# Kernel optimization log

Hardware: AMD Instinct MI355X
Metric: run time of the kernel (lower is better)

Reference implementation:

```python
import jax, jax.numpy as jnp
import numpy as np

B, H, NI, NT, D = 512, 1, 36, 50, 1024
NEG = -1e9
EPS = 1e-8

def setup_inputs() -> dict:
    key = jax.random.key(0)
    ks = jax.random.split(key, 12)
    s = 1.0 / np.sqrt(D)
    return {
        "imgE": jax.random.normal(ks[0], (B, H, NI, D), jnp.float32),
        "txtE": jax.random.normal(ks[1], (B, H, NT, D), jnp.float32),
        "x_mask": jax.random.randint(ks[2], (B, H, 1, NI), 0, 2).astype(bool),
        "y_mask": jax.random.randint(ks[3], (B, H, 1, NT), 0, 2).astype(bool),
        "W_img": jax.random.uniform(ks[4], (D, D), jnp.float32, -s, s),
        "b_img": jax.random.uniform(ks[5], (D,), jnp.float32, -s, s),
        "W_txt": jax.random.uniform(ks[6], (D, D), jnp.float32, -s, s),
        "b_txt": jax.random.uniform(ks[7], (D,), jnp.float32, -s, s),
        "W_img1": jax.random.uniform(ks[8], (D, D), jnp.float32, -s, s),
        "b_img1": jax.random.uniform(ks[9], (D,), jnp.float32, -s, s),
        "W_txt1": jax.random.uniform(ks[10], (D, D), jnp.float32, -s, s),
        "b_txt1": jax.random.uniform(ks[11], (D,), jnp.float32, -s, s),
    }

def reference(imgE, txtE, x_mask, y_mask,
              W_img, b_img, W_txt, b_txt, W_img1, b_img1, W_txt1, b_txt1):
    # projections
    x = jnp.einsum('bhnd,de->bhne', imgE, W_img) + b_img   # [B,H,NI,D]
    y = jnp.einsum('bhmd,de->bhme', txtE, W_txt) + b_txt   # [B,H,NT,D]
    # cosine-normalized attention scores [B,H,NI,NT]
    att = jnp.einsum('bhnd,bhmd->bhnm', x, y)
    wx = jnp.linalg.norm(x, axis=-1)[..., :, None]          # [B,H,NI,1]
    wy = jnp.linalg.norm(y, axis=-1)[..., None, :]          # [B,H,1,NT]
    att = att / jnp.maximum(wx * wy, EPS)
    # img <- txt direction
    att1 = jax.nn.softmax(jnp.where(y_mask, NEG, att), axis=-1)
    att_x = jnp.einsum('bhnm,bhmd->bhnd', att1, txtE)
    gate_x = jax.nn.sigmoid(att_x * imgE)
    fuse_x = jnp.einsum('bhnd,de->bhne', gate_x * att_x, W_img1) + b_img1
    img_out = fuse_x + imgE
    # txt <- img direction
    att2 = jax.nn.softmax(jnp.where(x_mask, NEG, jnp.swapaxes(att, 2, 3)), axis=-1)
    att_y = jnp.einsum('bhmn,bhnd->bhmd', att2, imgE)
    gate_y = jax.nn.sigmoid(att_y * txtE)
    fuse_y = jnp.einsum('bhmd,de->bhme', gate_y * att_y, W_txt1) + b_txt1
    txt_out = fuse_y + txtE
    return (img_out, txt_out)
```

## Files before the change

kernel.cpp:

```cpp
#include <hip/hip_runtime.h>

typedef unsigned short u16;
typedef unsigned int u32;
typedef __attribute__((ext_vector_type(8))) short sv8;
typedef __attribute__((ext_vector_type(4))) float fv4;

__device__ __forceinline__ u16 f2b(float f) {
  u32 u = __builtin_bit_cast(u32, f);
  u32 r = (u + 0x7fffu + ((u >> 16) & 1u)) >> 16;
  return (u16)r;
}
__device__ __forceinline__ float b2f(u16 h) {
  return __builtin_bit_cast(float, ((u32)h) << 16);
}
__device__ __forceinline__ void gld16(const void* g, void* l) {
  __builtin_amdgcn_global_load_lds(
      (const __attribute__((address_space(1))) u32*)g,
      (__attribute__((address_space(3))) u32*)l, 16, 0, 0);
}

__global__ __launch_bounds__(256) void cast_k(const float4* __restrict__ in,
                                              u16* __restrict__ out, int n4) {
  int i = blockIdx.x * 256 + threadIdx.x;
  const int stride = gridDim.x * 256;
  for (; i < n4; i += stride) {
    float4 v = in[i];
    u32 p0 = (u32)f2b(v.x) | ((u32)f2b(v.y) << 16);
    u32 p1 = (u32)f2b(v.z) | ((u32)f2b(v.w) << 16);
    uint2 o; o.x = p0; o.y = p1;
    ((uint2*)out)[i] = o;
  }
}

__global__ __launch_bounds__(256) void wtrans_k(const float* __restrict__ W0,
                                                const float* __restrict__ W1,
                                                const float* __restrict__ W2,
                                                const float* __restrict__ W3,
                                                u16* __restrict__ out) {
  const int z = blockIdx.z;
  const float* W = (z == 0) ? W0 : (z == 1) ? W1 : (z == 2) ? W2 : W3;
  u16* o = out + (size_t)z * 1048576;
  __shared__ float t[32][33];
  const int tid = threadIdx.x;
  const int r = tid >> 5, cc = tid & 31;
  const int d0 = blockIdx.x * 32, e0 = blockIdx.y * 32;
#pragma unroll
  for (int i = 0; i < 4; ++i)
    t[r + i * 8][cc] = W[(size_t)(d0 + r + i * 8) * 1024 + e0 + cc];
  __syncthreads();
#pragma unroll
  for (int i = 0; i < 4; ++i) {
    int row = r + i * 8;
    o[(size_t)(e0 + row) * 1024 + d0 + cc] = f2b(t[cc][row]);
  }
}

template <int MODE>
__global__ __launch_bounds__(512, 4) void gemm2_k(
    const u16* __restrict__ Aimg, const u16* __restrict__ Atxt,
    const u16* __restrict__ Wimg, const u16* __restrict__ Wtxt,
    const float* __restrict__ bii, const float* __restrict__ btt,
    const float* __restrict__ rii, const float* __restrict__ rtt,
    u16* __restrict__ obi, u16* __restrict__ obt,
    float* __restrict__ ofi, float* __restrict__ oft) {
  __shared__ __attribute__((aligned(16))) char smem[65536];
  const int tid = threadIdx.x;
  const int lane = tid & 63;
  const int w = tid >> 6;
  const int wm = w >> 2, wn = w & 3;
  const int l15 = lane & 15, l4 = lane >> 4;
  const int lin = blockIdx.y * 8 + blockIdx.x;
  const int xcd = lin & 7, slot = lin >> 3;
  const int bcol0 = (slot & 7) * 128;
  const int prow = xcd + ((slot >> 3) << 3);

  const char* Ab; const char* Bb; const float* bias; const float* resid;
  u16* ob; float* of; int brow0;
  if (prow < 144) {
    brow0 = prow * 128;
    Ab = (const char*)Aimg + (size_t)brow0 * 2048;
    Bb = (const char*)Wimg + (size_t)bcol0 * 2048;
    bias = bii; resid = rii; ob = obi; of = ofi;
  } else {
    brow0 = (prow - 144) * 128;
    Ab = (const char*)Atxt + (size_t)brow0 * 2048;
    Bb = (const char*)Wtxt + (size_t)bcol0 * 2048;
    bias = btt; resid = rtt; ob = obt; of = oft;
  }
  const int wr = wm * 64;
  const int wc = wn * 32;
  fv4 acc[4][2] = {};

  const int srow = tid >> 3;
  const int schunk = tid & 7;

  auto STAGE = [&](int bb, int k0) {
    char* base = smem + bb * 32768;
#pragma unroll
    for (int i = 0; i < 2; ++i) {
      int row = i * 64 + srow;
      int g = schunk ^ (row & 7);
      gld16(Ab + (size_t)row * 2048 + k0 * 2 + g * 16,
            base + i * 8192 + tid * 16);
    }
#pragma unroll
    for (int i = 0; i < 2; ++i) {
      int row = i * 64 + srow;
      int g = schunk ^ (row & 7);
      gld16(Bb + (size_t)row * 2048 + k0 * 2 + g * 16,
            base + 16384 + i * 8192 + tid * 16);
    }
  };

  STAGE(0, 0);
  for (int t = 0; t < 16; ++t) {
    const int cur = t & 1;
    if (t < 15) {
      STAGE(cur ^ 1, (t + 1) * 64);
      asm volatile("s_waitcnt vmcnt(4)" ::: "memory");
    } else {
      asm volatile("s_waitcnt vmcnt(0)" ::: "memory");
    }
    __builtin_amdgcn_s_barrier();
    __builtin_amdgcn_sched_barrier(0);
    const char* Al = smem + cur * 32768;
    const char* Bl = Al + 16384;
#pragma unroll
    for (int ks = 0; ks < 2; ++ks) {
      sv8 af[4], bf[2];
#pragma unroll
      for (int m = 0; m < 4; ++m) {
        int row = wr + m * 16 + l15;
        int c = (ks * 4 + l4) ^ (row & 7);
        af[m] = *(const sv8*)(Al + row * 128 + c * 16);
      }
#pragma unroll
      for (int n = 0; n < 2; ++n) {
        int row = wc + n * 16 + l15;
        int c = (ks * 4 + l4) ^ (row & 7);
        bf[n] = *(const sv8*)(Bl + row * 128 + c * 16);
      }
#pragma unroll
      for (int m = 0; m < 4; ++m)
#pragma unroll
        for (int n = 0; n < 2; ++n)
          acc[m][n] = __builtin_amdgcn_mfma_f32_16x16x32_bf16(af[m], bf[n], acc[m][n], 0, 0, 0);
    }
    __builtin_amdgcn_sched_barrier(0);
    __builtin_amdgcn_s_barrier();
  }

  float bv[2];
#pragma unroll
  for (int n = 0; n < 2; ++n) bv[n] = bias[bcol0 + wc + n * 16 + l15];
#pragma unroll
  for (int m = 0; m < 4; ++m) {
#pragma unroll
    for (int j = 0; j < 4; ++j) {
      const int row = brow0 + wr + m * 16 + l4 * 4 + j;
#pragma unroll
      for (int n = 0; n < 2; ++n) {
        const int col = bcol0 + wc + n * 16 + l15;
        const size_t idx = (size_t)row * 1024 + col;
        float r = acc[m][n][j] + bv[n];
        if (MODE == 0) {
          ob[idx] = f2b(r);
        } else {
          float rv = __builtin_nontemporal_load(&resid[idx]);
          __builtin_nontemporal_store(r + rv, &of[idx]);
        }
      }
    }
  }
}

__global__ __launch_bounds__(512) void score_k(const u16* __restrict__ Xb,
                                               const u16* __restrict__ Yb,
                                               const void* __restrict__ xmask,
                                               const void* __restrict__ ymask,
                                               float* __restrict__ P1g,
                                               float* __restrict__ P2g) {
  __shared__ float attL[48 * 65];
  __shared__ float wxL[88];
  __shared__ unsigned char msk[88];
  const int b = blockIdx.x;
  const int tid = threadIdx.x;
  const int w = tid >> 6, lane = tid & 63;
  const int l15 = lane & 15, l4 = lane >> 4;

  u32 det = 0;
  {
    const u32* mm = (const u32*)xmask;
#pragma unroll
    for (int i = 0; i < 16; ++i) det |= mm[i * 4];
    det |= mm[1] | mm[2] | mm[3];
  }
  const bool m_i32 = (det <= 1u);
  if (tid < 36)
    msk[tid] = (unsigned char)(m_i32 ? (((const int*)xmask)[b * 36 + tid] != 0)
                                     : (((const unsigned char*)xmask)[b * 36 + tid] != 0));
  if (tid >= 64 && tid < 114) {
    int m = tid - 64;
    msk[36 + m] = (unsigned char)(m_i32 ? (((const int*)ymask)[b * 50 + m] != 0)
                                        : (((const unsigned char*)ymask)[b * 50 + m] != 0));
  }

  const u16* Xr = Xb + (size_t)b * 36864;
  const u16* Yr = Yb + (size_t)b * 51200;

  if (w < 4) {
#pragma unroll
    for (int sweep = 0; sweep < 3; ++sweep) {
      int r = sweep * 32 + (tid >> 3);
      int j = tid & 7;
      if (r < 86) {
        const u32* p = (const u32*)((r < 36) ? (Xr + r * 1024)
                                             : (Yr + (size_t)(r - 36) * 1024)) + j * 64;
        float s = 0.f;
#pragma unroll
        for (int i = 0; i < 16; ++i) {
          uint4 q = ((const uint4*)p)[i];
          u32 qq[4] = {q.x, q.y, q.z, q.w};
#pragma unroll
          for (int k2 = 0; k2 < 4; ++k2) {
            float lo = __builtin_bit_cast(float, qq[k2] << 16);
            float hi = __builtin_bit_cast(float, qq[k2] & 0xffff0000u);
            s = fmaf(lo, lo, fmaf(hi, hi, s));
          }
        }
        s += __shfl_xor(s, 1); s += __shfl_xor(s, 2); s += __shfl_xor(s, 4);
        if (j == 0) wxL[r] = sqrtf(s);
      }
    }
  } else {
    const int tn = w - 4;
    fv4 ac0 = {}, ac1 = {}, ac2 = {};
    const u16* Yp = Yr + (size_t)(tn * 16 + l15) * 1024 + l4 * 8;
    const u16* Xp = Xr + (size_t)l15 * 1024 + l4 * 8;
#pragma unroll 2
    for (int ks = 0; ks < 32; ++ks) {
      sv8 bf = *(const sv8*)(Yp + ks * 32);
      sv8 a0 = *(const sv8*)(Xp + ks * 32);
      sv8 a1 = *(const sv8*)(Xp + 16 * 1024 + ks * 32);
      sv8 a2 = *(const sv8*)(Xp + 32 * 1024 + ks * 32);
      ac0 = __builtin_amdgcn_mfma_f32_16x16x32_bf16(a0, bf, ac0, 0, 0, 0);
      ac1 = __builtin_amdgcn_mfma_f32_16x16x32_bf16(a1, bf, ac1, 0, 0, 0);
      ac2 = __builtin_amdgcn_mfma_f32_16x16x32_bf16(a2, bf, ac2, 0, 0, 0);
    }
    const int col = tn * 16 + l15;
#pragma unroll
    for (int j = 0; j < 4; ++j) {
      attL[(l4 * 4 + j) * 65 + col] = ac0[j];
      attL[(16 + l4 * 4 + j) * 65 + col] = ac1[j];
      attL[(32 + l4 * 4 + j) * 65 + col] = ac2[j];
    }
  }
  __syncthreads();

#pragma unroll
  for (int sweep = 0; sweep < 2; ++sweep) {
    int R = sweep * 64 + (tid >> 3);
    int j = tid & 7;
    if (R < 36) {
      float wxn = wxL[R];
      float sv[7];
#pragma unroll
      for (int i = 0; i < 7; ++i) {
        int m = j + i * 8;
        if (m < 50) {
          float den = fmaxf(wxn * wxL[36 + m], 1e-8f);
          float v = attL[R * 65 + m] / den;
          sv[i] = msk[36 + m] ? -1e9f : v;
        } else sv[i] = -3.4e38f;
      }
      float mx = sv[0];
#pragma unroll
      for (int i = 1; i < 7; ++i) mx = fmaxf(mx, sv[i]);
      mx = fmaxf(mx, __shfl_xor(mx, 1));
      mx = fmaxf(mx, __shfl_xor(mx, 2));
      mx = fmaxf(mx, __shfl_xor(mx, 4));
      float e[7], sum = 0.f;
#pragma unroll
      for (int i = 0; i < 7; ++i) {
        e[i] = (j + i * 8 < 50) ? __expf(sv[i] - mx) : 0.f;
        sum += e[i];
      }
      sum += __shfl_xor(sum, 1); sum += __shfl_xor(sum, 2); sum += __shfl_xor(sum, 4);
      float rs = 1.f / sum;
      float* dst = P1g + ((size_t)b * 36 + R) * 64;
#pragma unroll
      for (int i = 0; i < 7; ++i) {
        int m = j + i * 8;
        if (m < 50) dst[m] = e[i] * rs;
      }
    } else if (R < 86) {
      int m = R - 36;
      float wym = wxL[R];
      float sv[5];
#pragma unroll
      for (int i = 0; i < 5; ++i) {
        int n = j + i * 8;
        if (n < 36) {
          float den = fmaxf(wxL[n] * wym, 1e-8f);
          float v = attL[n * 65 + m] / den;
          sv[i] = msk[n] ? -1e9f : v;
        } else sv[i] = -3.4e38f;
      }
      float mx = sv[0];
#pragma unroll
      for (int i = 1; i < 5; ++i) mx = fmaxf(mx, sv[i]);
      mx = fmaxf(mx, __shfl_xor(mx, 1));
      mx = fmaxf(mx, __shfl_xor(mx, 2));
      mx = fmaxf(mx, __shfl_xor(mx, 4));
      float e[5], sum = 0.f;
#pragma unroll
      for (int i = 0; i < 5; ++i) {
        e[i] = (j + i * 8 < 36) ? __expf(sv[i] - mx) : 0.f;
        sum += e[i];
      }
      sum += __shfl_xor(sum, 1); sum += __shfl_xor(sum, 2); sum += __shfl_xor(sum, 4);
      float rs = 1.f / sum;
      float* dst = P2g + ((size_t)b * 50 + m) * 64;
#pragma unroll
      for (int i = 0; i < 5; ++i) {
        int n = j + i * 8;
        if (n < 36) dst[n] = e[i] * rs;
      }
    }
  }
}

__global__ __launch_bounds__(256) void pv_k(const float* __restrict__ P1g,
                                            const float* __restrict__ P2g,
                                            const u16* __restrict__ imgA,
                                            const u16* __restrict__ txtA,
                                            u16* __restrict__ gxw,
                                            u16* __restrict__ gyw) {
  __shared__ float ldsP1[36 * 64];
  __shared__ float ldsP2[50 * 64];
  const int b = blockIdx.x & 511;
  const int d = ((blockIdx.x >> 9) << 8) + threadIdx.x;
  const int tid = threadIdx.x;

  {
    const float4* s1 = (const float4*)(P1g + (size_t)b * 2304);
    float4* l1 = (float4*)ldsP1;
    for (int i = tid; i < 576; i += 256) l1[i] = s1[i];
    const float4* s2 = (const float4*)(P2g + (size_t)b * 3200);
    float4* l2 = (float4*)ldsP2;
    for (int i = tid; i < 800; i += 256) l2[i] = s2[i];
  }

  const u16* tp = txtA + (size_t)b * 51200 + d;
  const u16* ip = imgA + (size_t)b * 36864 + d;
  float tv[50], iv[36];
#pragma unroll
  for (int m = 0; m < 50; ++m) tv[m] = b2f(tp[(size_t)m * 1024]);
#pragma unroll
  for (int n = 0; n < 36; ++n) iv[n] = b2f(ip[(size_t)n * 1024]);
  __syncthreads();

  u16* gx = gxw + (size_t)b * 36864 + d;
#pragma unroll
  for (int n = 0; n < 36; ++n) {
    const float4* pr4 = (const float4*)(ldsP1 + n * 64);
    float4 a4 = {0.f, 0.f, 0.f, 0.f};
#pragma unroll
    for (int i = 0; i < 12; ++i) {
      float4 p = pr4[i];
      a4.x = fmaf(p.x, tv[4 * i + 0], a4.x);
      a4.y = fmaf(p.y, tv[4 * i + 1], a4.y);
      a4.z = fmaf(p.z, tv[4 * i + 2], a4.z);
      a4.w = fmaf(p.w, tv[4 * i + 3], a4.w);
    }
    float acc = (a4.x + a4.y) + (a4.z + a4.w);
    acc = fmaf(ldsP1[n * 64 + 48], tv[48], acc);
    acc = fmaf(ldsP1[n * 64 + 49], tv[49], acc);
    float t = acc * iv[n];
    float g = acc / (1.f + __expf(-t));
    gx[(size_t)n * 1024] = f2b(g);
  }
  u16* gy = gyw + (size_t)b * 51200 + d;
#pragma unroll
  for (int m = 0; m < 50; ++m) {
    const float4* pr4 = (const float4*)(ldsP2 + m * 64);
    float4 a4 = {0.f, 0.f, 0.f, 0.f};
#pragma unroll
    for (int i = 0; i < 9; ++i) {
      float4 p = pr4[i];
      a4.x = fmaf(p.x, iv[4 * i + 0], a4.x);
      a4.y = fmaf(p.y, iv[4 * i + 1], a4.y);
      a4.z = fmaf(p.z, iv[4 * i + 2], a4.z);
      a4.w = fmaf(p.w, iv[4 * i + 3], a4.w);
    }
    float acc = (a4.x + a4.y) + (a4.z + a4.w);
    float t = acc * tv[m];
    float g = acc / (1.f + __expf(-t));
    gy[(size_t)m * 1024] = f2b(g);
  }
}

extern "C" void kernel_launch(void* const* d_in, const int* in_sizes, int n_in,
                              void* d_out, int out_size, void* d_ws, size_t ws_size,
                              hipStream_t stream) {
  (void)in_sizes; (void)n_in; (void)out_size; (void)ws_size;
  const float* imgE = (const float*)d_in[0];
  const float* txtE = (const float*)d_in[1];
  const void* xmask = d_in[2];
  const void* ymask = d_in[3];
  const float* W_img  = (const float*)d_in[4];
  const float* b_img  = (const float*)d_in[5];
  const float* W_txt  = (const float*)d_in[6];
  const float* b_txt  = (const float*)d_in[7];
  const float* W_img1 = (const float*)d_in[8];
  const float* b_img1 = (const float*)d_in[9];
  const float* W_txt1 = (const float*)d_in[10];
  const float* b_txt1 = (const float*)d_in[11];
  float* out_img = (float*)d_out;
  float* out_txt = out_img + (size_t)18874368;

  char* ws = (char*)d_ws;
  u16* Wt   = (u16*)(ws);
  u16* imgA = (u16*)(ws + 8388608);
  u16* txtA = (u16*)(ws + 46137344);
  u16* Xb   = (u16*)(ws + 98566144);
  u16* Yb   = (u16*)(ws + 136314880);
  float* P1g = (float*)(ws + 188743680);
  float* P2g = (float*)(ws + 193462272);
  u16* gxw  = (u16*)(ws + 98566144);
  u16* gyw  = (u16*)(ws + 136314880);

  cast_k<<<2048, 256, 0, stream>>>((const float4*)imgE, imgA, 4718592);
  cast_k<<<2048, 256, 0, stream>>>((const float4*)txtE, txtA, 6553600);
  wtrans_k<<<dim3(32, 32, 4), 256, 0, stream>>>(W_img, W_txt, W_img1, W_txt1, Wt);
  gemm2_k<0><<<dim3(8, 344), 512, 0, stream>>>(
      imgA, txtA, Wt, Wt + 1048576, b_img, b_txt, nullptr, nullptr,
      Xb, Yb, nullptr, nullptr);
  score_k<<<512, 512, 0, stream>>>(Xb, Yb, xmask, ymask, P1g, P2g);
  pv_k<<<2048, 256, 0, stream>>>(P1g, P2g, imgA, txtA, gxw, gyw);
  gemm2_k<1><<<dim3(8, 344), 512, 0, stream>>>(
      gxw, gyw, Wt + 2097152, Wt + 3145728, b_img1, b_txt1, imgE, txtE,
      nullptr, nullptr, out_img, out_txt);
}
```

Baseline: 414.4 us.

## Fuse score and PV kernels, merge cast launches, prefetch residual before GEMM loop

Merges the score/softmax kernel and the P·V gating kernel into one per-batch kernel that keeps the softmax probabilities in LDS, so they no longer round-trip through global memory. The two cast launches become one, and the output GEMM loads its residual tile into registers before the K loop so that latency overlaps with compute. The fused kernel runs only 512 blocks and covers D in two serial passes, which gives less parallelism than the old 2048-block PV kernel. The residual prefetch adds 32 registers per thread and may hurt GEMM occupancy.

New measurement: 622.1 us. 50.1% more time.

```diff
diff --git a/kernel.cpp b/kernel.cpp
--- a/kernel.cpp
+++ b/kernel.cpp
@@ -19,16 +19,22 @@
       (__attribute__((address_space(3))) u32*)l, 16, 0, 0);
 }
 
-__global__ __launch_bounds__(256) void cast_k(const float4* __restrict__ in,
-                                              u16* __restrict__ out, int n4) {
+__global__ __launch_bounds__(256) void cast2_k(const float4* __restrict__ inI,
+                                               const float4* __restrict__ inT,
+                                               u16* __restrict__ outI,
+                                               u16* __restrict__ outT,
+                                               int n4img, int n4tot) {
   int i = blockIdx.x * 256 + threadIdx.x;
   const int stride = gridDim.x * 256;
-  for (; i < n4; i += stride) {
-    float4 v = in[i];
+  for (; i < n4tot; i += stride) {
+    const float4* in = (i < n4img) ? inI : inT;
+    u16* out = (i < n4img) ? outI : outT;
+    int k = (i < n4img) ? i : i - n4img;
+    float4 v = in[k];
     u32 p0 = (u32)f2b(v.x) | ((u32)f2b(v.y) << 16);
     u32 p1 = (u32)f2b(v.z) | ((u32)f2b(v.w) << 16);
     uint2 o; o.x = p0; o.y = p1;
-    ((uint2*)out)[i] = o;
+    ((uint2*)out)[k] = o;
   }
 }
 
@@ -91,6 +97,21 @@
   const int wc = wn * 32;
   fv4 acc[4][2] = {};
 
+  float rv[4][4][2];
+  if (MODE == 1) {
+#pragma unroll
+    for (int m = 0; m < 4; ++m)
+#pragma unroll
+      for (int j = 0; j < 4; ++j)
+#pragma unroll
+        for (int n = 0; n < 2; ++n) {
+          const int row = brow0 + wr + m * 16 + l4 * 4 + j;
+          const int col = bcol0 + wc + n * 16 + l15;
+          rv[m][j][n] =
+              __builtin_nontemporal_load(&resid[(size_t)row * 1024 + col]);
+        }
+  }
+
   const int srow = tid >> 3;
   const int schunk = tid & 7;
 
@@ -166,23 +187,26 @@
         if (MODE == 0) {
           ob[idx] = f2b(r);
         } else {
-          float rv = __builtin_nontemporal_load(&resid[idx]);
-          __builtin_nontemporal_store(r + rv, &of[idx]);
+          __builtin_nontemporal_store(r + rv[m][j][n], &of[idx]);
         }
       }
     }
   }
 }
 
-__global__ __launch_bounds__(512) void score_k(const u16* __restrict__ Xb,
-                                               const u16* __restrict__ Yb,
-                                               const void* __restrict__ xmask,
-                                               const void* __restrict__ ymask,
-                                               float* __restrict__ P1g,
-                                               float* __restrict__ P2g) {
+__global__ __launch_bounds__(512, 2) void attn2_k(const u16* __restrict__ Xb,
+                                                  const u16* __restrict__ Yb,
+                                                  const u16* __restrict__ imgA,
+                                                  const u16* __restrict__ txtA,
+                                                  const void* __restrict__ xmask,
+                                                  const void* __restrict__ ymask,
+                                                  u16* __restrict__ gxw,
+                                                  u16* __restrict__ gyw) {
   __shared__ float attL[48 * 65];
   __shared__ float wxL[88];
   __shared__ unsigned char msk[88];
+  __shared__ float P1L[36 * 64];
+  __shared__ float P2L[50 * 64];
   const int b = blockIdx.x;
   const int tid = threadIdx.x;
   const int w = tid >> 6, lane = tid & 63;
@@ -287,11 +311,10 @@
       }
       sum += __shfl_xor(sum, 1); sum += __shfl_xor(sum, 2); sum += __shfl_xor(sum, 4);
       float rs = 1.f / sum;
-      float* dst = P1g + ((size_t)b * 36 + R) * 64;
 #pragma unroll
       for (int i = 0; i < 7; ++i) {
         int m = j + i * 8;
-        if (m < 50) dst[m] = e[i] * rs;
+        if (m < 50) P1L[R * 64 + m] = e[i] * rs;
       }
     } else if (R < 86) {
       int m = R - 36;
@@ -320,83 +343,64 @@
       }
       sum += __shfl_xor(sum, 1); sum += __shfl_xor(sum, 2); sum += __shfl_xor(sum, 4);
       float rs = 1.f / sum;
-      float* dst = P2g + ((size_t)b * 50 + m) * 64;
 #pragma unroll
       for (int i = 0; i < 5; ++i) {
         int n = j + i * 8;
-        if (n < 36) dst[n] = e[i] * rs;
-      }
-    }
-  }
-}
-
-__global__ __launch_bounds__(256) void pv_k(const float* __restrict__ P1g,
-                                            const float* __restrict__ P2g,
-                                            const u16* __restrict__ imgA,
-                                            const u16* __restrict__ txtA,
-                                            u16* __restrict__ gxw,
-                                            u16* __restrict__ gyw) {
-  __shared__ float ldsP1[36 * 64];
-  __shared__ float ldsP2[50 * 64];
-  const int b = blockIdx.x & 511;
-  const int d = ((blockIdx.x >> 9) << 8) + threadIdx.x;
-  const int tid = threadIdx.x;
-
-  {
-    const float4* s1 = (const float4*)(P1g + (size_t)b * 2304);
-    float4* l1 = (float4*)ldsP1;
-    for (int i = tid; i < 576; i += 256) l1[i] = s1[i];
-    const float4* s2 = (const float4*)(P2g + (size_t)b * 3200);
-    float4* l2 = (float4*)ldsP2;
-    for (int i = tid; i < 800; i += 256) l2[i] = s2[i];
-  }
-
-  const u16* tp = txtA + (size_t)b * 51200 + d;
-  const u16* ip = imgA + (size_t)b * 36864 + d;
-  float tv[50], iv[36];
-#pragma unroll
-  for (int m = 0; m < 50; ++m) tv[m] = b2f(tp[(size_t)m * 1024]);
-#pragma unroll
-  for (int n = 0; n < 36; ++n) iv[n] = b2f(ip[(size_t)n * 1024]);
+        if (n < 36) P2L[m * 64 + n] = e[i] * rs;
+      }
+    }
+  }
   __syncthreads();
 
-  u16* gx = gxw + (size_t)b * 36864 + d;
-#pragma unroll
-  for (int n = 0; n < 36; ++n) {
-    const float4* pr4 = (const float4*)(ldsP1 + n * 64);
-    float4 a4 = {0.f, 0.f, 0.f, 0.f};
-#pragma unroll
-    for (int i = 0; i < 12; ++i) {
-      float4 p = pr4[i];
-      a4.x = fmaf(p.x, tv[4 * i + 0], a4.x);
-      a4.y = fmaf(p.y, tv[4 * i + 1], a4.y);
-      a4.z = fmaf(p.z, tv[4 * i + 2], a4.z);
-      a4.w = fmaf(p.w, tv[4 * i + 3], a4.w);
-    }
-    float acc = (a4.x + a4.y) + (a4.z + a4.w);
-    acc = fmaf(ldsP1[n * 64 + 48], tv[48], acc);
-    acc = fmaf(ldsP1[n * 64 + 49], tv[49], acc);
-    float t = acc * iv[n];
-    float g = acc / (1.f + __expf(-t));
-    gx[(size_t)n * 1024] = f2b(g);
-  }
-  u16* gy = gyw + (size_t)b * 51200 + d;
-#pragma unroll
-  for (int m = 0; m < 50; ++m) {
-    const float4* pr4 = (const float4*)(ldsP2 + m * 64);
-    float4 a4 = {0.f, 0.f, 0.f, 0.f};
-#pragma unroll
-    for (int i = 0; i < 9; ++i) {
-      float4 p = pr4[i];
-      a4.x = fmaf(p.x, iv[4 * i + 0], a4.x);
-      a4.y = fmaf(p.y, iv[4 * i + 1], a4.y);
-      a4.z = fmaf(p.z, iv[4 * i + 2], a4.z);
-      a4.w = fmaf(p.w, iv[4 * i + 3], a4.w);
-    }
-    float acc = (a4.x + a4.y) + (a4.z + a4.w);
-    float t = acc * tv[m];
-    float g = acc / (1.f + __expf(-t));
-    gy[(size_t)m * 1024] = f2b(g);
+#pragma unroll 1
+  for (int rep = 0; rep < 2; ++rep) {
+    const int d = rep * 512 + tid;
+    const u16* tp = txtA + (size_t)b * 51200 + d;
+    const u16* ip = imgA + (size_t)b * 36864 + d;
+    float tv[50], iv[36];
+#pragma unroll
+    for (int m = 0; m < 50; ++m) tv[m] = b2f(tp[(size_t)m * 1024]);
+#pragma unroll
+    for (int n = 0; n < 36; ++n) iv[n] = b2f(ip[(size_t)n * 1024]);
+
+    u16* gx = gxw + (size_t)b * 36864 + d;
+#pragma unroll
+    for (int n = 0; n < 36; ++n) {
+      const float4* pr4 = (const float4*)(P1L + n * 64);
+      float4 a4 = {0.f, 0.f, 0.f, 0.f};
+#pragma unroll
+      for (int i = 0; i < 12; ++i) {
+        float4 p = pr4[i];
+        a4.x = fmaf(p.x, tv[4 * i + 0], a4.x);
+        a4.y = fmaf(p.y, tv[4 * i + 1], a4.y);
+        a4.z = fmaf(p.z, tv[4 * i + 2], a4.z);
+        a4.w = fmaf(p.w, tv[4 * i + 3], a4.w);
+      }
+      float acc = (a4.x + a4.y) + (a4.z + a4.w);
+      acc = fmaf(P1L[n * 64 + 48], tv[48], acc);
+      acc = fmaf(P1L[n * 64 + 49], tv[49], acc);
+      float t = acc * iv[n];
+      float g = acc / (1.f + __expf(-t));
+      gx[(size_t)n * 1024] = f2b(g);
+    }
+    u16* gy = gyw + (size_t)b * 51200 + d;
+#pragma unroll
+    for (int m = 0; m < 50; ++m) {
+      const float4* pr4 = (const float4*)(P2L + m * 64);
+      float4 a4 = {0.f, 0.f, 0.f, 0.f};
+#pragma unroll
+      for (int i = 0; i < 9; ++i) {
+        float4 p = pr4[i];
+        a4.x = fmaf(p.x, iv[4 * i + 0], a4.x);
+        a4.y = fmaf(p.y, iv[4 * i + 1], a4.y);
+        a4.z = fmaf(p.z, iv[4 * i + 2], a4.z);
+        a4.w = fmaf(p.w, iv[4 * i + 3], a4.w);
+      }
+      float acc = (a4.x + a4.y) + (a4.z + a4.w);
+      float t = acc * tv[m];
+      float g = acc / (1.f + __expf(-t));
+      gy[(size_t)m * 1024] = f2b(g);
+    }
   }
 }
 
@@ -425,19 +429,16 @@
   u16* txtA = (u16*)(ws + 46137344);
   u16* Xb   = (u16*)(ws + 98566144);
   u16* Yb   = (u16*)(ws + 136314880);
-  float* P1g = (float*)(ws + 188743680);
-  float* P2g = (float*)(ws + 193462272);
-  u16* gxw  = (u16*)(ws + 98566144);
-  u16* gyw  = (u16*)(ws + 136314880);
-
-  cast_k<<<2048, 256, 0, stream>>>((const float4*)imgE, imgA, 4718592);
-  cast_k<<<2048, 256, 0, stream>>>((const float4*)txtE, txtA, 6553600);
+  u16* gxw  = (u16*)(ws + 188743680);
+  u16* gyw  = (u16*)(ws + 226492416);
+
+  cast2_k<<<2048, 256, 0, stream>>>((const float4*)imgE, (const float4*)txtE,
+                                    imgA, txtA, 4718592, 11272192);
   wtrans_k<<<dim3(32, 32, 4), 256, 0, stream>>>(W_img, W_txt, W_img1, W_txt1, Wt);
   gemm2_k<0><<<dim3(8, 344), 512, 0, stream>>>(
       imgA, txtA, Wt, Wt + 1048576, b_img, b_txt, nullptr, nullptr,
       Xb, Yb, nullptr, nullptr);
-  score_k<<<512, 512, 0, stream>>>(Xb, Yb, xmask, ymask, P1g, P2g);
-  pv_k<<<2048, 256, 0, stream>>>(P1g, P2g, imgA, txtA, gxw, gyw);
+  attn2_k<<<512, 512, 0, stream>>>(Xb, Yb, imgA, txtA, xmask, ymask, gxw, gyw);
   gemm2_k<1><<<dim3(8, 344), 512, 0, stream>>>(
       gxw, gyw, Wt + 2097152, Wt + 3145728, b_img1, b_txt1, imgE, txtE,
       nullptr, nullptr, out_img, out_txt);
```
